# Kernel optimization log

Measured on AMD Instinct MI355X. Metric: run time of the kernel, lower is better.

The kernel has to match this reference:

```python
import jax, jax.numpy as jnp
import numpy as np

HIDDEN_DIM = 2048
NUM_EXPERTS = 8
TOP_K = 2
SCORE_SCALE_FACTOR = 1.0
TOKENS = 8192  # batch_size in the original 2D input


def setup_inputs() -> dict:
    key = jax.random.key(0)
    k1, k2, k3 = jax.random.split(key, 3)
    hidden_states = jax.random.normal(k1, (TOKENS, HIDDEN_DIM), dtype=jnp.float32)
    # nn.Linear weights (out_features, in_features), Kaiming-uniform-like scale
    gate_w = jax.random.normal(k2, (NUM_EXPERTS, HIDDEN_DIM), dtype=jnp.float32) / np.float32(np.sqrt(HIDDEN_DIM))
    expert_w = jax.random.normal(k3, (NUM_EXPERTS, HIDDEN_DIM, HIDDEN_DIM), dtype=jnp.float32) / np.float32(np.sqrt(HIDDEN_DIM))
    return {"hidden_states": hidden_states, "gate_w": gate_w, "expert_w": expert_w}


def reference(hidden_states, gate_w, expert_w):
    # router: logits = x @ W_gate^T, softmax in float32 (matches F.softmax(dtype=torch.float))
    router_logits = hidden_states @ gate_w.T                      # [T, E]
    routing_probs = jax.nn.softmax(router_logits.astype(jnp.float32), axis=-1)
    top_w, top_i = jax.lax.top_k(routing_probs, TOP_K)            # [T, K]
    top_w = top_w / jnp.sum(top_w, axis=-1, keepdims=True)        # renormalize over top-k
    top_w = top_w.astype(hidden_states.dtype)

    T = hidden_states.shape[0]
    # dense combine weights [T, E]: zero for unselected experts -> exactly the
    # gather-GEMM-scatter math (full capacity, no dropped tokens)
    combine = jnp.zeros((T, NUM_EXPERTS), dtype=hidden_states.dtype)
    combine = combine.at[jnp.arange(T)[:, None], top_i].set(top_w)

    # out[t,h] = scale * sum_e combine[t,e] * (x[t,:] @ expert_w[e]^T)[h]
    final_hidden_states = jnp.einsum('td,ehd,te->th', hidden_states, expert_w, combine) * SCORE_SCALE_FACTOR
    return final_hidden_states, router_logits
```

## Files before the change

kernel.cpp:

```cpp
#include <hip/hip_runtime.h>
#include <hip/hip_bf16.h>
#include <stdint.h>

#define TOKENS 8192
#define HD     2048
#define NE     8

typedef __attribute__((ext_vector_type(8))) short short8;
typedef __attribute__((ext_vector_type(8))) unsigned short ushort8v;
typedef __attribute__((ext_vector_type(4))) float f32x4;

__device__ __forceinline__ unsigned short f2bf_rne(float f) {
  union { float f; unsigned u; } v; v.f = f;
  unsigned u = v.u;
  return (unsigned short)((u + 0x7fffu + ((u >> 16) & 1u)) >> 16);
}

__device__ __forceinline__ void async_load16(const void* g, void* lds) {
  __builtin_amdgcn_global_load_lds(
      (const __attribute__((address_space(1))) unsigned int*)g,
      (__attribute__((address_space(3))) unsigned int*)lds, 16, 0, 0);
}

__global__ void convert_w_kernel(const float* __restrict__ src,
                                 unsigned short* __restrict__ dst, int n8) {
  int i = blockIdx.x * blockDim.x + threadIdx.x;
  int stride = gridDim.x * blockDim.x;
  const float4* s4 = (const float4*)src;
  ushort8v* d8 = (ushort8v*)dst;
  for (; i < n8; i += stride) {
    float4 a = s4[i * 2], b = s4[i * 2 + 1];
    ushort8v o;
    o[0] = f2bf_rne(a.x); o[1] = f2bf_rne(a.y);
    o[2] = f2bf_rne(a.z); o[3] = f2bf_rne(a.w);
    o[4] = f2bf_rne(b.x); o[5] = f2bf_rne(b.y);
    o[6] = f2bf_rne(b.z); o[7] = f2bf_rne(b.w);
    d8[i] = o;
  }
}

__global__ __launch_bounds__(256) void router_kernel(
    const float* __restrict__ x, const float* __restrict__ gw,
    unsigned short* __restrict__ xb, float* __restrict__ logits_out) {
  const int wid  = threadIdx.x >> 6;
  const int lane = threadIdx.x & 63;
  const int t = blockIdx.x * 4 + wid;

  const float4* xr = (const float4*)(x + (size_t)t * HD);
  const float4* g4 = (const float4*)gw;
  ushort4* xb4 = (ushort4*)(xb + (size_t)t * HD);

  float acc[NE];
#pragma unroll
  for (int e = 0; e < NE; ++e) acc[e] = 0.f;

#pragma unroll
  for (int it = 0; it < 8; ++it) {
    int idx = it * 64 + lane;
    float4 v = xr[idx];
    ushort4 o;
    o.x = f2bf_rne(v.x); o.y = f2bf_rne(v.y);
    o.z = f2bf_rne(v.z); o.w = f2bf_rne(v.w);
    xb4[idx] = o;
#pragma unroll
    for (int e = 0; e < NE; ++e) {
      float4 g = g4[e * 512 + idx];
      acc[e] += v.x * g.x + v.y * g.y + v.z * g.z + v.w * g.w;
    }
  }
#pragma unroll
  for (int e = 0; e < NE; ++e) {
#pragma unroll
    for (int off = 32; off > 0; off >>= 1)
      acc[e] += __shfl_xor(acc[e], off, 64);
  }
  if (lane == 0) {
    float* lo = logits_out + (size_t)t * NE;
#pragma unroll
    for (int e = 0; e < NE; ++e) lo[e] = acc[e];
  }
}

__global__ __launch_bounds__(1024) void bucket_kernel(
    const float* __restrict__ logits, int* __restrict__ counts,
    int* __restrict__ btok, float* __restrict__ bwt) {
  const int e = blockIdx.x;
  __shared__ int lcount;
  if (threadIdx.x == 0) lcount = 0;
  __syncthreads();
  const int lane = threadIdx.x & 63;

  for (int base = 0; base < TOKENS; base += 1024) {
    int t = base + threadIdx.x;
    const float* lo = logits + (size_t)t * NE;
    float l[NE];
#pragma unroll
    for (int k = 0; k < NE; ++k) l[k] = lo[k];
    int i0 = 0; float b0 = l[0];
#pragma unroll
    for (int k = 1; k < NE; ++k) if (l[k] > b0) { b0 = l[k]; i0 = k; }
    int i1 = -1; float b1 = -3.4e38f;
#pragma unroll
    for (int k = 0; k < NE; ++k) if (k != i0 && l[k] > b1) { b1 = l[k]; i1 = k; }
    float w0 = 1.f / (1.f + __expf(b1 - b0));
    float w1 = 1.f - w0;
#pragma unroll
    for (int s = 0; s < 2; ++s) {
      int  ex = s ? i1 : i0;
      float w = s ? w1 : w0;
      bool p = (ex == e);
      unsigned long long mask = __ballot(p);
      int prefix = __popcll(mask & ((1ull << lane) - 1ull));
      int tot    = __popcll(mask);
      int wb = 0;
      if (lane == 0 && tot) wb = atomicAdd(&lcount, tot);
      wb = __shfl(wb, 0, 64);
      if (p) {
        btok[e * TOKENS + wb + prefix] = t;
        bwt [e * TOKENS + wb + prefix] = w;
      }
    }
  }
  __syncthreads();
  if (threadIdx.x == 0) counts[e * 32] = lcount;
}

__global__ __launch_bounds__(256, 4) void moe_gemm_kernel(
    const unsigned short* __restrict__ xb,
    const unsigned short* __restrict__ wb,
    const int* __restrict__ counts,
    const int* __restrict__ btok,
    const float* __restrict__ bwt,
    float* __restrict__ out) {
  int d = blockIdx.x;
  int e, coltile, rowtile;
  if (d < 2048) {
    e       = d & 7;
    rowtile = (d >> 3) & 15;
    coltile = d >> 7;
  } else {
    int u = d - 2048;
    rowtile = 16 + (u >> 7);
    coltile = (u & 127) >> 3;
    e       = u & 7;
  }
  const int cnt = counts[e * 32];
  if (rowtile * 128 >= cnt) return;

  __shared__ unsigned short As[128 * 64];
  __shared__ unsigned short Bs[128 * 64];

  const int tid  = threadIdx.x;
  const int wid  = tid >> 6;
  const int lane = tid & 63;

  int a_off[4], b_off[4];
#pragma unroll
  for (int it = 0; it < 4; ++it) {
    int slot = wid * 256 + it * 64 + lane;
    int row  = slot >> 3;
    int ch   = (slot & 7) ^ (row & 7);
    int rc   = rowtile * 128 + row;
    rc = rc < cnt ? rc : cnt - 1;
    a_off[it] = btok[e * TOKENS + rc] * HD + ch * 8;
    b_off[it] = (e * HD + coltile * 128 + row) * HD + ch * 8;
  }

  f32x4 acc[4][4];
#pragma unroll
  for (int i = 0; i < 4; ++i)
#pragma unroll
    for (int j = 0; j < 4; ++j) acc[i][j] = (f32x4){0.f, 0.f, 0.f, 0.f};

  const int quad = lane >> 4;
  const int mrow = lane & 15;
  const int wm2  = wid >> 1;
  const int wn2  = wid & 1;

  int a_rd[2][4], b_rd[2][4];
#pragma unroll
  for (int h = 0; h < 2; ++h)
#pragma unroll
    for (int i = 0; i < 4; ++i) {
      int ra = wm2 * 64 + i * 16 + mrow;
      a_rd[h][i] = ra * 64 + ((4 * h + quad) ^ (ra & 7)) * 8;
      int rb = wn2 * 64 + i * 16 + mrow;
      b_rd[h][i] = rb * 64 + ((4 * h + quad) ^ (rb & 7)) * 8;
    }

  for (int k0 = 0; k0 < HD; k0 += 64) {
#pragma unroll
    for (int it = 0; it < 4; ++it) {
      async_load16(xb + a_off[it] + k0, &As[(wid * 256 + it * 64) * 8]);
      async_load16(wb + b_off[it] + k0, &Bs[(wid * 256 + it * 64) * 8]);
    }
    __syncthreads();
#pragma unroll
    for (int h = 0; h < 2; ++h) {
      short8 fa[4], fb[4];
#pragma unroll
      for (int i = 0; i < 4; ++i) {
        fa[i] = *(const short8*)&As[a_rd[h][i]];
        fb[i] = *(const short8*)&Bs[b_rd[h][i]];
      }
#pragma unroll
      for (int i = 0; i < 4; ++i)
#pragma unroll
        for (int j = 0; j < 4; ++j)
          acc[i][j] = __builtin_amdgcn_mfma_f32_16x16x32_bf16(
              fa[i], fb[j], acc[i][j], 0, 0, 0);
    }
    __syncthreads();
  }

#pragma unroll
  for (int i = 0; i < 4; ++i)
#pragma unroll
    for (int r = 0; r < 4; ++r) {
      int m  = wm2 * 64 + i * 16 + quad * 4 + r;
      int gm = rowtile * 128 + m;
      if (gm < cnt) {
        int   tok = btok[e * TOKENS + gm];
        float w   = bwt [e * TOKENS + gm];
        float* orow = out + (size_t)tok * HD + coltile * 128 + wn2 * 64 + mrow;
#pragma unroll
        for (int j = 0; j < 4; ++j)
          unsafeAtomicAdd(orow + j * 16, w * acc[i][j][r]);
      }
    }
}

extern "C" void kernel_launch(void* const* d_in, const int* in_sizes, int n_in,
                              void* d_out, int out_size, void* d_ws, size_t ws_size,
                              hipStream_t stream) {
  const float* x  = (const float*)d_in[0];
  const float* gw = (const float*)d_in[1];
  const float* ew = (const float*)d_in[2];
  float* out = (float*)d_out;

  char* ws = (char*)d_ws;
  unsigned short* xb = (unsigned short*)ws;
  unsigned short* wb = (unsigned short*)(ws + 33554432u);
  int*   counts = (int*)(ws + 100663296u);
  int*   btok   = (int*)(ws + 100664320u);
  float* bwt    = (float*)(ws + 100926464u);

  float* logits = out + (size_t)TOKENS * HD;

  hipMemsetAsync(out, 0, (size_t)TOKENS * HD * sizeof(float), stream);
  convert_w_kernel<<<4096, 256, 0, stream>>>(ew, wb, NE * HD * HD / 8);
  router_kernel<<<TOKENS / 4, 256, 0, stream>>>(x, gw, xb, logits);
  bucket_kernel<<<NE, 1024, 0, stream>>>(logits, counts, btok, bwt);
  moe_gemm_kernel<<<8192, 256, 0, stream>>>(xb, wb, counts, btok, bwt, out);
}
```

Before: 496.1 us.

## Fuse expert weight bf16 conversion into the MoE GEMM's LDS read path

Drops the separate kernel that converted the fp32 expert weights to bf16. The GEMM now streams fp32 weight tiles straight into LDS with a 16-chunk swizzle and packs them to bf16 by truncation at fragment-read time. This avoids a full read and write pass over the weights and one launch. In exchange it doubles the B-tile bytes read per block, doubles B's LDS footprint (occupancy hint lowered from 4 to 3), and switches weight rounding from round-to-nearest-even to round-toward-zero. The launch grid shrinks to 4096 blocks, which caps each expert at 32 row tiles.

```diff
diff --git a/kernel.cpp b/kernel.cpp
--- a/kernel.cpp
+++ b/kernel.cpp
@@ -7,7 +7,6 @@
 #define NE     8
 
 typedef __attribute__((ext_vector_type(8))) short short8;
-typedef __attribute__((ext_vector_type(8))) unsigned short ushort8v;
 typedef __attribute__((ext_vector_type(4))) float f32x4;
 
 __device__ __forceinline__ unsigned short f2bf_rne(float f) {
@@ -22,21 +21,13 @@
       (__attribute__((address_space(3))) unsigned int*)lds, 16, 0, 0);
 }
 
-__global__ void convert_w_kernel(const float* __restrict__ src,
-                                 unsigned short* __restrict__ dst, int n8) {
-  int i = blockIdx.x * blockDim.x + threadIdx.x;
-  int stride = gridDim.x * blockDim.x;
-  const float4* s4 = (const float4*)src;
-  ushort8v* d8 = (ushort8v*)dst;
-  for (; i < n8; i += stride) {
-    float4 a = s4[i * 2], b = s4[i * 2 + 1];
-    ushort8v o;
-    o[0] = f2bf_rne(a.x); o[1] = f2bf_rne(a.y);
-    o[2] = f2bf_rne(a.z); o[3] = f2bf_rne(a.w);
-    o[4] = f2bf_rne(b.x); o[5] = f2bf_rne(b.y);
-    o[6] = f2bf_rne(b.z); o[7] = f2bf_rne(b.w);
-    d8[i] = o;
-  }
+__device__ __forceinline__ short8 pack8_bf16_rtz(f32x4 a, f32x4 b) {
+  union { short8 s; unsigned u[4]; } r;
+  r.u[0] = __builtin_amdgcn_perm(__float_as_uint(a[1]), __float_as_uint(a[0]), 0x07060302u);
+  r.u[1] = __builtin_amdgcn_perm(__float_as_uint(a[3]), __float_as_uint(a[2]), 0x07060302u);
+  r.u[2] = __builtin_amdgcn_perm(__float_as_uint(b[1]), __float_as_uint(b[0]), 0x07060302u);
+  r.u[3] = __builtin_amdgcn_perm(__float_as_uint(b[3]), __float_as_uint(b[2]), 0x07060302u);
+  return r.s;
 }
 
 __global__ __launch_bounds__(256) void router_kernel(
@@ -125,9 +116,9 @@
   if (threadIdx.x == 0) counts[e * 32] = lcount;
 }
 
-__global__ __launch_bounds__(256, 4) void moe_gemm_kernel(
+__global__ __launch_bounds__(256, 3) void moe_gemm_kernel(
     const unsigned short* __restrict__ xb,
-    const unsigned short* __restrict__ wb,
+    const float* __restrict__ ew,
     const int* __restrict__ counts,
     const int* __restrict__ btok,
     const float* __restrict__ bwt,
@@ -140,21 +131,21 @@
     coltile = d >> 7;
   } else {
     int u = d - 2048;
+    e       = u & 7;
+    coltile = (u >> 3) & 15;
     rowtile = 16 + (u >> 7);
-    coltile = (u & 127) >> 3;
-    e       = u & 7;
   }
   const int cnt = counts[e * 32];
   if (rowtile * 128 >= cnt) return;
 
   __shared__ unsigned short As[128 * 64];
-  __shared__ unsigned short Bs[128 * 64];
+  __shared__ float          Bs[128 * 64];
 
   const int tid  = threadIdx.x;
   const int wid  = tid >> 6;
   const int lane = tid & 63;
 
-  int a_off[4], b_off[4];
+  int a_off[4];
 #pragma unroll
   for (int it = 0; it < 4; ++it) {
     int slot = wid * 256 + it * 64 + lane;
@@ -163,7 +154,14 @@
     int rc   = rowtile * 128 + row;
     rc = rc < cnt ? rc : cnt - 1;
     a_off[it] = btok[e * TOKENS + rc] * HD + ch * 8;
-    b_off[it] = (e * HD + coltile * 128 + row) * HD + ch * 8;
+  }
+  int b_off[8];
+#pragma unroll
+  for (int it = 0; it < 8; ++it) {
+    int slot = wid * 512 + it * 64 + lane;
+    int row  = slot >> 4;
+    int ch   = (slot & 15) ^ (row & 15);
+    b_off[it] = (e * HD + coltile * 128 + row) * HD + ch * 4;
   }
 
   f32x4 acc[4][4];
@@ -177,7 +175,8 @@
   const int wm2  = wid >> 1;
   const int wn2  = wid & 1;
 
-  int a_rd[2][4], b_rd[2][4];
+  int a_rd[2][4];
+  int b_rd[2][4][2];
 #pragma unroll
   for (int h = 0; h < 2; ++h)
 #pragma unroll
@@ -185,15 +184,18 @@
       int ra = wm2 * 64 + i * 16 + mrow;
       a_rd[h][i] = ra * 64 + ((4 * h + quad) ^ (ra & 7)) * 8;
       int rb = wn2 * 64 + i * 16 + mrow;
-      b_rd[h][i] = rb * 64 + ((4 * h + quad) ^ (rb & 7)) * 8;
+      int c0 = h * 8 + quad * 2;
+      b_rd[h][i][0] = rb * 64 + (c0       ^ (rb & 15)) * 4;
+      b_rd[h][i][1] = rb * 64 + ((c0 + 1) ^ (rb & 15)) * 4;
     }
 
   for (int k0 = 0; k0 < HD; k0 += 64) {
 #pragma unroll
-    for (int it = 0; it < 4; ++it) {
+    for (int it = 0; it < 4; ++it)
       async_load16(xb + a_off[it] + k0, &As[(wid * 256 + it * 64) * 8]);
-      async_load16(wb + b_off[it] + k0, &Bs[(wid * 256 + it * 64) * 8]);
-    }
+#pragma unroll
+    for (int it = 0; it < 8; ++it)
+      async_load16(ew + b_off[it] + k0, &Bs[(wid * 512 + it * 64) * 4]);
     __syncthreads();
 #pragma unroll
     for (int h = 0; h < 2; ++h) {
@@ -201,7 +203,9 @@
 #pragma unroll
       for (int i = 0; i < 4; ++i) {
         fa[i] = *(const short8*)&As[a_rd[h][i]];
-        fb[i] = *(const short8*)&Bs[b_rd[h][i]];
+        f32x4 g0 = *(const f32x4*)&Bs[b_rd[h][i][0]];
+        f32x4 g1 = *(const f32x4*)&Bs[b_rd[h][i][1]];
+        fb[i] = pack8_bf16_rtz(g0, g1);
       }
 #pragma unroll
       for (int i = 0; i < 4; ++i)
@@ -240,16 +244,14 @@
 
   char* ws = (char*)d_ws;
   unsigned short* xb = (unsigned short*)ws;
-  unsigned short* wb = (unsigned short*)(ws + 33554432u);
-  int*   counts = (int*)(ws + 100663296u);
-  int*   btok   = (int*)(ws + 100664320u);
-  float* bwt    = (float*)(ws + 100926464u);
+  int*   counts = (int*)(ws + 33554432u);
+  int*   btok   = (int*)(ws + 33555456u);
+  float* bwt    = (float*)(ws + 33817600u);
 
   float* logits = out + (size_t)TOKENS * HD;
 
   hipMemsetAsync(out, 0, (size_t)TOKENS * HD * sizeof(float), stream);
-  convert_w_kernel<<<4096, 256, 0, stream>>>(ew, wb, NE * HD * HD / 8);
   router_kernel<<<TOKENS / 4, 256, 0, stream>>>(x, gw, xb, logits);
   bucket_kernel<<<NE, 1024, 0, stream>>>(logits, counts, btok, bwt);
-  moe_gemm_kernel<<<8192, 256, 0, stream>>>(xb, wb, counts, btok, bwt, out);
-}
+  moe_gemm_kernel<<<4096, 256, 0, stream>>>(xb, ew, counts, btok, bwt, out);
+}
```

After: 521.7 us. +5.2%, slower.

## Replace atomic scatter with slot-tagged direct stores plus bf16 combine pass

Applied to the files above, without the earlier changes.

Each token's routing slot is now encoded in the bucket token index. The GEMM epilogue writes the first-slot contribution straight into the fp32 output and the second-slot contribution into a bf16 side buffer, which a new combine kernel adds in afterwards. This removes the output memset and the fp32 atomic adds. The change also merges the weight conversion and router kernels into one launch and switches the MFMA from 16x16x32 to 32x32x16 tiles. In exchange, the second expert's contribution is rounded to bf16, and the GEMM grid is halved, so it only covers up to 4096 tokens per expert, which assumes fairly balanced routing.

```diff
diff --git a/kernel.cpp b/kernel.cpp
--- a/kernel.cpp
+++ b/kernel.cpp
@@ -6,9 +6,10 @@
 #define HD     2048
 #define NE     8
 
-typedef __attribute__((ext_vector_type(8))) short short8;
-typedef __attribute__((ext_vector_type(8))) unsigned short ushort8v;
-typedef __attribute__((ext_vector_type(4))) float f32x4;
+typedef __attribute__((ext_vector_type(8)))  short short8;
+typedef __attribute__((ext_vector_type(8)))  unsigned short ushort8v;
+typedef __attribute__((ext_vector_type(4)))  float f32x4;
+typedef __attribute__((ext_vector_type(16))) float f32x16;
 
 __device__ __forceinline__ unsigned short f2bf_rne(float f) {
   union { float f; unsigned u; } v; v.f = f;
@@ -22,26 +23,27 @@
       (__attribute__((address_space(3))) unsigned int*)lds, 16, 0, 0);
 }
 
-__global__ void convert_w_kernel(const float* __restrict__ src,
-                                 unsigned short* __restrict__ dst, int n8) {
-  int i = blockIdx.x * blockDim.x + threadIdx.x;
-  int stride = gridDim.x * blockDim.x;
-  const float4* s4 = (const float4*)src;
-  ushort8v* d8 = (ushort8v*)dst;
-  for (; i < n8; i += stride) {
-    float4 a = s4[i * 2], b = s4[i * 2 + 1];
-    ushort8v o;
-    o[0] = f2bf_rne(a.x); o[1] = f2bf_rne(a.y);
-    o[2] = f2bf_rne(a.z); o[3] = f2bf_rne(a.w);
-    o[4] = f2bf_rne(b.x); o[5] = f2bf_rne(b.y);
-    o[6] = f2bf_rne(b.z); o[7] = f2bf_rne(b.w);
-    d8[i] = o;
-  }
-}
-
-__global__ __launch_bounds__(256) void router_kernel(
+__global__ __launch_bounds__(256) void prep_kernel(
     const float* __restrict__ x, const float* __restrict__ gw,
-    unsigned short* __restrict__ xb, float* __restrict__ logits_out) {
+    const float* __restrict__ ew, unsigned short* __restrict__ xb,
+    unsigned short* __restrict__ wb, float* __restrict__ logits_out) {
+  if (blockIdx.x >= 2048) {
+    int i = (blockIdx.x - 2048) * 256 + threadIdx.x;
+    const int n8 = NE * HD * HD / 8;
+    const int stride = 4096 * 256;
+    const float4* s4 = (const float4*)ew;
+    ushort8v* d8 = (ushort8v*)wb;
+    for (; i < n8; i += stride) {
+      float4 a = s4[i * 2], b = s4[i * 2 + 1];
+      ushort8v o;
+      o[0] = f2bf_rne(a.x); o[1] = f2bf_rne(a.y);
+      o[2] = f2bf_rne(a.z); o[3] = f2bf_rne(a.w);
+      o[4] = f2bf_rne(b.x); o[5] = f2bf_rne(b.y);
+      o[6] = f2bf_rne(b.z); o[7] = f2bf_rne(b.w);
+      d8[i] = o;
+    }
+    return;
+  }
   const int wid  = threadIdx.x >> 6;
   const int lane = threadIdx.x & 63;
   const int t = blockIdx.x * 4 + wid;
@@ -116,7 +118,7 @@
       if (lane == 0 && tot) wb = atomicAdd(&lcount, tot);
       wb = __shfl(wb, 0, 64);
       if (p) {
-        btok[e * TOKENS + wb + prefix] = t;
+        btok[e * TOKENS + wb + prefix] = t | (s << 13);
         bwt [e * TOKENS + wb + prefix] = w;
       }
     }
@@ -131,7 +133,8 @@
     const int* __restrict__ counts,
     const int* __restrict__ btok,
     const float* __restrict__ bwt,
-    float* __restrict__ out) {
+    float* __restrict__ out,
+    unsigned short* __restrict__ slot1) {
   int d = blockIdx.x;
   int e, coltile, rowtile;
   if (d < 2048) {
@@ -140,9 +143,9 @@
     coltile = d >> 7;
   } else {
     int u = d - 2048;
+    e       = u & 7;
+    coltile = (u & 127) >> 3;
     rowtile = 16 + (u >> 7);
-    coltile = (u & 127) >> 3;
-    e       = u & 7;
   }
   const int cnt = counts[e * 32];
   if (rowtile * 128 >= cnt) return;
@@ -162,30 +165,32 @@
     int ch   = (slot & 7) ^ (row & 7);
     int rc   = rowtile * 128 + row;
     rc = rc < cnt ? rc : cnt - 1;
-    a_off[it] = btok[e * TOKENS + rc] * HD + ch * 8;
+    a_off[it] = (btok[e * TOKENS + rc] & (TOKENS - 1)) * HD + ch * 8;
     b_off[it] = (e * HD + coltile * 128 + row) * HD + ch * 8;
   }
 
-  f32x4 acc[4][4];
-#pragma unroll
-  for (int i = 0; i < 4; ++i)
-#pragma unroll
-    for (int j = 0; j < 4; ++j) acc[i][j] = (f32x4){0.f, 0.f, 0.f, 0.f};
-
-  const int quad = lane >> 4;
-  const int mrow = lane & 15;
-  const int wm2  = wid >> 1;
-  const int wn2  = wid & 1;
+  f32x16 acc[2][2];
+#pragma unroll
+  for (int i = 0; i < 2; ++i)
+#pragma unroll
+    for (int j = 0; j < 2; ++j)
+#pragma unroll
+      for (int r = 0; r < 16; ++r) acc[i][j][r] = 0.f;
+
+  const int l5  = lane >> 5;
+  const int ln  = lane & 31;
+  const int wm2 = wid >> 1;
+  const int wn2 = wid & 1;
 
   int a_rd[2][4], b_rd[2][4];
 #pragma unroll
-  for (int h = 0; h < 2; ++h)
-#pragma unroll
-    for (int i = 0; i < 4; ++i) {
-      int ra = wm2 * 64 + i * 16 + mrow;
-      a_rd[h][i] = ra * 64 + ((4 * h + quad) ^ (ra & 7)) * 8;
-      int rb = wn2 * 64 + i * 16 + mrow;
-      b_rd[h][i] = rb * 64 + ((4 * h + quad) ^ (rb & 7)) * 8;
+  for (int t = 0; t < 2; ++t)
+#pragma unroll
+    for (int kc = 0; kc < 4; ++kc) {
+      int ra = wm2 * 64 + t * 32 + ln;
+      a_rd[t][kc] = ra * 64 + ((kc * 2 + l5) ^ (ra & 7)) * 8;
+      int rb = wn2 * 64 + t * 32 + ln;
+      b_rd[t][kc] = rb * 64 + ((kc * 2 + l5) ^ (rb & 7)) * 8;
     }
 
   for (int k0 = 0; k0 < HD; k0 += 64) {
@@ -195,39 +200,65 @@
       async_load16(wb + b_off[it] + k0, &Bs[(wid * 256 + it * 64) * 8]);
     }
     __syncthreads();
-#pragma unroll
-    for (int h = 0; h < 2; ++h) {
-      short8 fa[4], fb[4];
-#pragma unroll
-      for (int i = 0; i < 4; ++i) {
-        fa[i] = *(const short8*)&As[a_rd[h][i]];
-        fb[i] = *(const short8*)&Bs[b_rd[h][i]];
+    short8 fa[2][4], fb[2][4];
+#pragma unroll
+    for (int t = 0; t < 2; ++t)
+#pragma unroll
+      for (int kc = 0; kc < 4; ++kc) {
+        fa[t][kc] = *(const short8*)&As[a_rd[t][kc]];
+        fb[t][kc] = *(const short8*)&Bs[b_rd[t][kc]];
       }
 #pragma unroll
-      for (int i = 0; i < 4; ++i)
-#pragma unroll
-        for (int j = 0; j < 4; ++j)
-          acc[i][j] = __builtin_amdgcn_mfma_f32_16x16x32_bf16(
-              fa[i], fb[j], acc[i][j], 0, 0, 0);
-    }
+    for (int kc = 0; kc < 4; ++kc)
+#pragma unroll
+      for (int i = 0; i < 2; ++i)
+#pragma unroll
+        for (int j = 0; j < 2; ++j)
+          acc[i][j] = __builtin_amdgcn_mfma_f32_32x32x16_bf16(
+              fa[i][kc], fb[j][kc], acc[i][j], 0, 0, 0);
     __syncthreads();
   }
 
 #pragma unroll
-  for (int i = 0; i < 4; ++i)
-#pragma unroll
-    for (int r = 0; r < 4; ++r) {
-      int m  = wm2 * 64 + i * 16 + quad * 4 + r;
-      int gm = rowtile * 128 + m;
+  for (int ti = 0; ti < 2; ++ti)
+#pragma unroll
+    for (int rg = 0; rg < 16; ++rg) {
+      int row = (rg & 3) + 8 * (rg >> 2) + 4 * l5;
+      int gm  = rowtile * 128 + wm2 * 64 + ti * 32 + row;
       if (gm < cnt) {
-        int   tok = btok[e * TOKENS + gm];
-        float w   = bwt [e * TOKENS + gm];
-        float* orow = out + (size_t)tok * HD + coltile * 128 + wn2 * 64 + mrow;
-#pragma unroll
-        for (int j = 0; j < 4; ++j)
-          unsafeAtomicAdd(orow + j * 16, w * acc[i][j][r]);
+        int   dv = btok[e * TOKENS + gm];
+        float w  = bwt [e * TOKENS + gm];
+        int   nb = coltile * 128 + wn2 * 64 + ln;
+        float v0 = w * acc[ti][0][rg];
+        float v1 = w * acc[ti][1][rg];
+        if (dv < TOKENS) {
+          float* orow = out + (size_t)dv * HD + nb;
+          orow[0]  = v0;
+          orow[32] = v1;
+        } else {
+          unsigned short* srow = slot1 + (size_t)(dv - TOKENS) * HD + nb;
+          srow[0]  = f2bf_rne(v0);
+          srow[32] = f2bf_rne(v1);
+        }
       }
     }
+}
+
+__global__ __launch_bounds__(256) void combine_kernel(
+    const unsigned short* __restrict__ s1, float* __restrict__ out) {
+  size_t u = (size_t)blockIdx.x * 256 + threadIdx.x;
+  ushort8v sv = ((const ushort8v*)s1)[u];
+  float4* o = (float4*)out + u * 2;
+  float4 a = o[0], b = o[1];
+  a.x += __uint_as_float((unsigned)sv[0] << 16);
+  a.y += __uint_as_float((unsigned)sv[1] << 16);
+  a.z += __uint_as_float((unsigned)sv[2] << 16);
+  a.w += __uint_as_float((unsigned)sv[3] << 16);
+  b.x += __uint_as_float((unsigned)sv[4] << 16);
+  b.y += __uint_as_float((unsigned)sv[5] << 16);
+  b.z += __uint_as_float((unsigned)sv[6] << 16);
+  b.w += __uint_as_float((unsigned)sv[7] << 16);
+  o[0] = a; o[1] = b;
 }
 
 extern "C" void kernel_launch(void* const* d_in, const int* in_sizes, int n_in,
@@ -239,17 +270,17 @@
   float* out = (float*)d_out;
 
   char* ws = (char*)d_ws;
-  unsigned short* xb = (unsigned short*)ws;
-  unsigned short* wb = (unsigned short*)(ws + 33554432u);
-  int*   counts = (int*)(ws + 100663296u);
-  int*   btok   = (int*)(ws + 100664320u);
-  float* bwt    = (float*)(ws + 100926464u);
+  unsigned short* xb    = (unsigned short*)ws;
+  unsigned short* wb    = (unsigned short*)(ws + 33554432u);
+  unsigned short* slot1 = (unsigned short*)(ws + 100663296u);
+  int*   counts = (int*)(ws + 134217728u);
+  int*   btok   = (int*)(ws + 134218752u);
+  float* bwt    = (float*)(ws + 134480896u);
 
   float* logits = out + (size_t)TOKENS * HD;
 
-  hipMemsetAsync(out, 0, (size_t)TOKENS * HD * sizeof(float), stream);
-  convert_w_kernel<<<4096, 256, 0, stream>>>(ew, wb, NE * HD * HD / 8);
-  router_kernel<<<TOKENS / 4, 256, 0, stream>>>(x, gw, xb, logits);
+  prep_kernel<<<6144, 256, 0, stream>>>(x, gw, ew, xb, wb, logits);
   bucket_kernel<<<NE, 1024, 0, stream>>>(logits, counts, btok, bwt);
-  moe_gemm_kernel<<<8192, 256, 0, stream>>>(xb, wb, counts, btok, bwt, out);
-}
+  moe_gemm_kernel<<<4096, 256, 0, stream>>>(xb, wb, counts, btok, bwt, out, slot1);
+  combine_kernel<<<8192, 256, 0, stream>>>(slot1, out);
+}
```

After: 473.9 us. 4.5% less time.
